# Kernel optimization log

Hardware: AMD Instinct MI355X
Metric: run time of the kernel (lower is better)

Reference implementation:

```python
import jax, jax.numpy as jnp
import numpy as np

N_EMBD = 768
N_HEAD = 12
HEAD_DIM = N_EMBD // N_HEAD
EPS = 1e-6


def setup_inputs() -> dict:
    key = jax.random.key(0)
    ks = jax.random.split(key, 8)
    B, T, C = 4, 2048, N_EMBD
    s = 0.02
    return {
        "x": jax.random.normal(ks[0], (B, T, C), jnp.float32),
        "ln1_w": jnp.ones((C,), jnp.float32),
        "ln1_b": jnp.zeros((C,), jnp.float32),
        "W_attn": jax.random.normal(ks[1], (C, 3 * C), jnp.float32) * s,
        "b_attn": jnp.zeros((3 * C,), jnp.float32),
        "W_attn_proj": jax.random.normal(ks[2], (C, C), jnp.float32) * s,
        "b_attn_proj": jnp.zeros((C,), jnp.float32),
        "ln2_w": jnp.ones((C,), jnp.float32),
        "ln2_b": jnp.zeros((C,), jnp.float32),
        "W_fc": jax.random.normal(ks[3], (C, 4 * C), jnp.float32) * s,
        "b_fc": jnp.zeros((4 * C,), jnp.float32),
        "W_mlp_proj": jax.random.normal(ks[4], (4 * C, C), jnp.float32) * s,
        "b_mlp_proj": jnp.zeros((C,), jnp.float32),
    }


def layer_norm(x, w, b):
    # Faithful to MyLayerNorm: (x - mean) / (std + eps), std with ddof=0
    mean = jnp.mean(x, axis=-1, keepdims=True)
    std = jnp.sqrt(jnp.mean((x - mean) ** 2, axis=-1, keepdims=True))
    return w * (x - mean) / (std + EPS) + b


def attention(h, W_attn, b_attn, W_proj, b_proj):
    B, T, C = h.shape
    qkv = h @ W_attn + b_attn                      # [B,T,3C]
    q, k, v = jnp.split(qkv, 3, axis=-1)
    # [B,T,C] -> [B,H,T,D]
    def to_heads(t):
        return t.reshape(B, T, N_HEAD, HEAD_DIM).transpose(0, 2, 1, 3)
    q, k, v = to_heads(q), to_heads(k), to_heads(v)
    att = jnp.einsum("bhtd,bhsd->bhts", q, k) * (1.0 / np.sqrt(HEAD_DIM))
    causal = jnp.tril(jnp.ones((T, T), bool))[None, None]
    att = jnp.where(causal, att, -jnp.inf)
    att = jax.nn.softmax(att, axis=-1)
    y = jnp.einsum("bhts,bhsd->bhtd", att, v)      # [B,H,T,D]
    y = y.transpose(0, 2, 1, 3).reshape(B, T, C)
    return y @ W_proj + b_proj


def mlp(h, W_fc, b_fc, W_proj, b_proj):
    h = jax.nn.gelu(h @ W_fc + b_fc, approximate=False)
    return h @ W_proj + b_proj


def reference(x, ln1_w, ln1_b, W_attn, b_attn, W_attn_proj, b_attn_proj,
              ln2_w, ln2_b, W_fc, b_fc, W_mlp_proj, b_mlp_proj):
    x = x + attention(layer_norm(x, ln1_w, ln1_b), W_attn, b_attn, W_attn_proj, b_attn_proj)
    x = x + mlp(layer_norm(x, ln2_w, ln2_b), W_fc, b_fc, W_mlp_proj, b_mlp_proj)
    return x
```

## Files before the change

### kernel.cpp

```cpp
#include <hip/hip_runtime.h>
#include <hip/hip_bf16.h>
#include <math.h>

#define N_EMBD 768
#define N_HEAD 12
#define HEAD_DIM 64
#define TOKENS 8192
#define SEQ 2048
#define BATCH 4
#define NQT (SEQ / 64)

typedef __attribute__((ext_vector_type(8))) short short8;
typedef __attribute__((ext_vector_type(4))) short short4v;
typedef __attribute__((ext_vector_type(4))) float f32x4;

__device__ __forceinline__ short f2bf(float f) {
    unsigned u = __builtin_bit_cast(unsigned, f);
    unsigned r = (u + 0x7fffu + ((u >> 16) & 1u)) >> 16;
    return (short)r;
}
__device__ __forceinline__ short f2bf_fast(float f) {
    unsigned u = __builtin_bit_cast(unsigned, f);
    return (short)((u + 0x8000u) >> 16);
}

__device__ __forceinline__ float gelu_fast(float x) {
    float z = 1.5957691216057308f * x * (1.0f + 0.044715f * x * x);
    return x / (1.0f + __expf(-z));
}

__device__ __forceinline__ void gld16(const void* g, void* l) {
    __builtin_amdgcn_global_load_lds(
        (const __attribute__((address_space(1))) unsigned int*)g,
        (__attribute__((address_space(3))) unsigned int*)l, 16, 0, 0);
}

__global__ __launch_bounds__(256) void wT_all(
        const float* __restrict__ Wa, short* __restrict__ Ta,
        const float* __restrict__ Wp, short* __restrict__ Tp,
        const float* __restrict__ Wf, short* __restrict__ Tf,
        const float* __restrict__ Wm, short* __restrict__ Tm) {
    __shared__ float T[32][33];
    int id = blockIdx.x;
    const float* W; short* Wt; int K, N;
    if (id < 1728)      { W = Wa; Wt = Ta; K = 768;  N = 2304; }
    else if (id < 2304) { W = Wp; Wt = Tp; K = 768;  N = 768;  id -= 1728; }
    else if (id < 4608) { W = Wf; Wt = Tf; K = 768;  N = 3072; id -= 2304; }
    else                { W = Wm; Wt = Tm; K = 3072; N = 768;  id -= 4608; }
    int tn = N >> 5;
    int n0 = (id % tn) * 32, k0 = (id / tn) * 32;
    int c = threadIdx.x & 31, r0 = threadIdx.x >> 5;
#pragma unroll
    for (int i = 0; i < 32; i += 8)
        T[r0 + i][c] = W[(size_t)(k0 + r0 + i) * N + n0 + c];
    __syncthreads();
#pragma unroll
    for (int i = 0; i < 32; i += 8)
        Wt[(size_t)(n0 + r0 + i) * K + k0 + c] = f2bf(T[c][r0 + i]);
}

__global__ __launch_bounds__(256) void ln_bf_kernel(const float* __restrict__ x,
                                                    const float* __restrict__ w,
                                                    const float* __restrict__ b,
                                                    short* __restrict__ out) {
    int row = blockIdx.x * 4 + (threadIdx.x >> 6);
    int lane = threadIdx.x & 63;
    const float4* xr = (const float4*)(x + (size_t)row * N_EMBD);
    const float4* wr = (const float4*)w;
    const float4* br = (const float4*)b;

    float4 v[3];
#pragma unroll
    for (int i = 0; i < 3; ++i) v[i] = xr[lane + 64 * i];
    float s = 0.f;
#pragma unroll
    for (int i = 0; i < 3; ++i) s += v[i].x + v[i].y + v[i].z + v[i].w;
#pragma unroll
    for (int off = 1; off < 64; off <<= 1) s += __shfl_xor(s, off, 64);
    float mean = s * (1.f / 768.f);

    float var = 0.f;
#pragma unroll
    for (int i = 0; i < 3; ++i) {
        float a0 = v[i].x - mean, a1 = v[i].y - mean,
              a2 = v[i].z - mean, a3 = v[i].w - mean;
        var += a0 * a0 + a1 * a1 + a2 * a2 + a3 * a3;
    }
#pragma unroll
    for (int off = 1; off < 64; off <<= 1) var += __shfl_xor(var, off, 64);
    float inv = 1.f / (sqrtf(var * (1.f / 768.f)) + 1e-6f);

    short4v* yr = (short4v*)(out + (size_t)row * N_EMBD);
#pragma unroll
    for (int i = 0; i < 3; ++i) {
        float4 wv = wr[lane + 64 * i], bv = br[lane + 64 * i];
        short4v o;
        o[0] = f2bf(wv.x * (v[i].x - mean) * inv + bv.x);
        o[1] = f2bf(wv.y * (v[i].y - mean) * inv + bv.y);
        o[2] = f2bf(wv.z * (v[i].z - mean) * inv + bv.z);
        o[3] = f2bf(wv.w * (v[i].w - mean) * inv + bv.w);
        yr[lane + 64 * i] = o;
    }
}

template <int ACT, int RES, int OUTBF, int VOUT>
__global__ __launch_bounds__(256) void gemm_mfma(
        const short* __restrict__ A,
        const short* __restrict__ Bt,
        const float* __restrict__ bias,
        const float* __restrict__ res,
        void* __restrict__ outp,
        short* __restrict__ vt,
        int M, int N, int K) {
    __shared__ short As[8192];
    __shared__ short Bs[8192];
    int tid = threadIdx.x;
    int wave = tid >> 6, lane = tid & 63;
    int quad = lane >> 4, l15 = lane & 15;
    int m0 = blockIdx.x * 128, n0 = blockIdx.y * 128;
    int wm = wave >> 1, wn = wave & 1;
    int sr = lane >> 2, sc = (lane & 3) * 8;

    f32x4 acc[4][4];
#pragma unroll
    for (int i = 0; i < 4; ++i)
#pragma unroll
        for (int j = 0; j < 4; ++j) acc[i][j] = (f32x4){0.f, 0.f, 0.f, 0.f};

    const short* ag = A + (size_t)(m0 + wave * 32 + sr) * K + sc;
    const short* bg = Bt + (size_t)(n0 + wave * 32 + sr) * K + sc;
    int woff = wave * 1024;

    gld16(ag, &As[woff]);
    gld16(ag + (size_t)16 * K, &As[woff + 512]);
    gld16(bg, &Bs[woff]);
    gld16(bg + (size_t)16 * K, &Bs[woff + 512]);

    int nk = K >> 5;
    for (int it = 0; it < nk; ++it) {
        int cb = (it & 1) * 4096;
        __syncthreads();
        if (it + 1 < nk) {
            int nb = ((it + 1) & 1) * 4096 + woff;
            int kn = (it + 1) << 5;
            gld16(ag + kn, &As[nb]);
            gld16(ag + kn + (size_t)16 * K, &As[nb + 512]);
            gld16(bg + kn, &Bs[nb]);
            gld16(bg + kn + (size_t)16 * K, &Bs[nb + 512]);
        }
        short8 af[4], bfr[4];
#pragma unroll
        for (int mt = 0; mt < 4; ++mt)
            af[mt] = *(const short8*)&As[cb + (wm * 64 + mt * 16 + l15) * 32 + quad * 8];
#pragma unroll
        for (int nt = 0; nt < 4; ++nt)
            bfr[nt] = *(const short8*)&Bs[cb + (wn * 64 + nt * 16 + l15) * 32 + quad * 8];
#pragma unroll
        for (int mt = 0; mt < 4; ++mt)
#pragma unroll
            for (int nt = 0; nt < 4; ++nt)
                acc[mt][nt] = __builtin_amdgcn_mfma_f32_16x16x32_bf16(
                    af[mt], bfr[nt], acc[mt][nt], 0, 0, 0);
    }

    if (VOUT && n0 >= 1536) {
#pragma unroll
        for (int mt = 0; mt < 4; ++mt) {
            int row0 = m0 + wm * 64 + mt * 16 + quad * 4;
            int b = row0 >> 11, t0 = row0 & 2047;
#pragma unroll
            for (int nt = 0; nt < 4; ++nt) {
                int col = n0 + wn * 64 + nt * 16 + l15;
                int vcol = col - 1536;
                int bh = b * N_HEAD + (vcol >> 6);
                int d = vcol & 63;
                float bi = bias[col];
                short4v o;
#pragma unroll
                for (int r = 0; r < 4; ++r) o[r] = f2bf(acc[mt][nt][r] + bi);
                *(short4v*)&vt[((size_t)bh * 64 + d) * SEQ + t0] = o;
            }
        }
        return;
    }

#pragma unroll
    for (int mt = 0; mt < 4; ++mt) {
        int row0 = m0 + wm * 64 + mt * 16 + quad * 4;
#pragma unroll
        for (int nt = 0; nt < 4; ++nt) {
            int col = n0 + wn * 64 + nt * 16 + l15;
            float bi = bias[col];
#pragma unroll
            for (int r = 0; r < 4; ++r) {
                float v = acc[mt][nt][r] + bi;
                if (ACT == 1) v = gelu_fast(v);
                if (RES) v += res[(size_t)(row0 + r) * N + col];
                if (OUTBF) ((short*)outp)[(size_t)(row0 + r) * N + col] = f2bf(v);
                else       ((float*)outp)[(size_t)(row0 + r) * N + col] = v;
            }
        }
    }
}

template <int ACT, int RES, int OUTBF>
__global__ __launch_bounds__(256) void gemm_mfma_n64(
        const short* __restrict__ A,
        const short* __restrict__ Bt,
        const float* __restrict__ bias,
        const float* __restrict__ res,
        void* __restrict__ outp,
        int M, int N, int K) {
    __shared__ short As[8192];
    __shared__ short Bs[4096];
    int tid = threadIdx.x;
    int wave = tid >> 6, lane = tid & 63;
    int quad = lane >> 4, l15 = lane & 15;
    int m0 = blockIdx.x * 128, n0 = blockIdx.y * 64;
    int wm = wave >> 1, wn = wave & 1;
    int sr = lane >> 2, sc = (lane & 3) * 8;

    f32x4 acc[4][2];
#pragma unroll
    for (int i = 0; i < 4; ++i)
#pragma unroll
        for (int j = 0; j < 2; ++j) acc[i][j] = (f32x4){0.f, 0.f, 0.f, 0.f};

    const short* gptr[3];
    int loff[3];
    bool isa[3];
#pragma unroll
    for (int j = 0; j < 3; ++j) {
        int c = wave * 3 + j;
        if (c < 8) {
            gptr[j] = A + (size_t)(m0 + c * 16 + sr) * K + sc;
            loff[j] = c * 512; isa[j] = true;
        } else {
            gptr[j] = Bt + (size_t)(n0 + (c - 8) * 16 + sr) * K + sc;
            loff[j] = (c - 8) * 512; isa[j] = false;
        }
    }

#pragma unroll
    for (int j = 0; j < 3; ++j)
        gld16(gptr[j], isa[j] ? &As[loff[j]] : &Bs[loff[j]]);

    int nk = K >> 5;
    for (int it = 0; it < nk; ++it) {
        int cba = (it & 1) * 4096, cbb = (it & 1) * 2048;
        __syncthreads();
        if (it + 1 < nk) {
            int nba = ((it + 1) & 1) * 4096, nbb = ((it + 1) & 1) * 2048;
            int kn = (it + 1) << 5;
#pragma unroll
            for (int j = 0; j < 3; ++j)
                gld16(gptr[j] + kn, isa[j] ? &As[nba + loff[j]] : &Bs[nbb + loff[j]]);
        }
        short8 af[4], bfr[2];
#pragma unroll
        for (int mt = 0; mt < 4; ++mt)
            af[mt] = *(const short8*)&As[cba + (wm * 64 + mt * 16 + l15) * 32 + quad * 8];
#pragma unroll
        for (int nt = 0; nt < 2; ++nt)
            bfr[nt] = *(const short8*)&Bs[cbb + (wn * 32 + nt * 16 + l15) * 32 + quad * 8];
#pragma unroll
        for (int mt = 0; mt < 4; ++mt)
#pragma unroll
            for (int nt = 0; nt < 2; ++nt)
                acc[mt][nt] = __builtin_amdgcn_mfma_f32_16x16x32_bf16(
                    af[mt], bfr[nt], acc[mt][nt], 0, 0, 0);
    }

#pragma unroll
    for (int mt = 0; mt < 4; ++mt) {
        int row0 = m0 + wm * 64 + mt * 16 + quad * 4;
#pragma unroll
        for (int nt = 0; nt < 2; ++nt) {
            int col = n0 + wn * 32 + nt * 16 + l15;
            float bi = bias[col];
#pragma unroll
            for (int r = 0; r < 4; ++r) {
                float v = acc[mt][nt][r] + bi;
                if (ACT == 1) v = gelu_fast(v);
                if (RES) v += res[(size_t)(row0 + r) * N + col];
                if (OUTBF) ((short*)outp)[(size_t)(row0 + r) * N + col] = f2bf(v);
                else       ((float*)outp)[(size_t)(row0 + r) * N + col] = v;
            }
        }
    }
}

__device__ __forceinline__ void attn_tile(
        const short* __restrict__ qkv, const short* __restrict__ Vt,
        short* __restrict__ y, int bh, int qt,
        short* Qs, short* Ks, short* Vs, short* Ps) {
    int tid = threadIdx.x;
    int wave = tid >> 6, lane = tid & 63;
    int quad = lane >> 4, l15 = lane & 15;
    int h = bh % N_HEAD, b = bh / N_HEAD;
    size_t bT = (size_t)b * SEQ;
    int q0 = qt * 64;
    int sr = lane >> 2, sc = (lane & 3) * 8;

    const short ONE_BF = (short)0x3F80;
    short8 ones;
#pragma unroll
    for (int j = 0; j < 8; ++j) ones[j] = ONE_BF;

    __syncthreads();
#pragma unroll
    for (int j = 0; j < 2; ++j) {
        int c = wave * 2 + j;
        int sub = c >> 2, r0 = (c & 3) * 16;
        const short* g = qkv + (bT + q0 + r0 + sr) * 2304 + h * 64 + sub * 32 + sc;
        gld16(g, &Qs[sub * 2048 + r0 * 32]);
    }
#pragma unroll
    for (int j = 0; j < 4; ++j) {
        int c = wave * 4 + j;
        if (c < 8) {
            int sub = c >> 2, r0 = (c & 3) * 16;
            const short* g = qkv + (bT + r0 + sr) * 2304 + 768 + h * 64 + sub * 32 + sc;
            gld16(g, &Ks[sub * 2048 + r0 * 32]);
        } else {
            int cv = c - 8;
            int sub = cv >> 2, r0 = (cv & 3) * 16;
            const short* g = Vt + ((size_t)bh * 64 + r0 + sr) * SEQ + sub * 32 + sc;
            gld16(g, &Vs[sub * 2048 + r0 * 32]);
        }
    }
    __syncthreads();
    short8 qf[2];
    qf[0] = *(const short8*)&Qs[(wave * 16 + l15) * 32 + quad * 8];
    qf[1] = *(const short8*)&Qs[2048 + (wave * 16 + l15) * 32 + quad * 8];

    f32x4 o[4];
#pragma unroll
    for (int nt = 0; nt < 4; ++nt) o[nt] = (f32x4){0.f, 0.f, 0.f, 0.f};
    f32x4 lacc = (f32x4){0.f, 0.f, 0.f, 0.f};

    for (int kt = 0; kt <= qt; ++kt) {
        int cb = (kt & 1) * 4096;
        if (kt) __syncthreads();
        if (kt < qt) {
            int nb = ((kt + 1) & 1) * 4096;
            int k0n = (kt + 1) * 64;
#pragma unroll
            for (int j = 0; j < 4; ++j) {
                int c = wave * 4 + j;
                if (c < 8) {
                    int sub = c >> 2, r0 = (c & 3) * 16;
                    const short* g = qkv + (bT + k0n + r0 + sr) * 2304 + 768 + h * 64 + sub * 32 + sc;
                    gld16(g, &Ks[nb + sub * 2048 + r0 * 32]);
                } else {
                    int cv = c - 8;
                    int sub = cv >> 2, r0 = (cv & 3) * 16;
                    const short* g = Vt + ((size_t)bh * 64 + r0 + sr) * SEQ + k0n + sub * 32 + sc;
                    gld16(g, &Vs[nb + sub * 2048 + r0 * 32]);
                }
            }
        }

        f32x4 sacc[4];
#pragma unroll
        for (int nt = 0; nt < 4; ++nt) sacc[nt] = (f32x4){0.f, 0.f, 0.f, 0.f};
#pragma unroll
        for (int nt = 0; nt < 4; ++nt)
#pragma unroll
            for (int ks = 0; ks < 2; ++ks) {
                short8 kf = *(const short8*)&Ks[cb + ks * 2048 + (nt * 16 + l15) * 32 + quad * 8];
                sacc[nt] = __builtin_amdgcn_mfma_f32_16x16x32_bf16(qf[ks], kf, sacc[nt], 0, 0, 0);
            }

        bool diag = (kt == qt);
#pragma unroll
        for (int nt = 0; nt < 4; ++nt) {
            int scol = nt * 16 + l15;
            int base = (scol >> 5) * 2048 + (scol & 31);
#pragma unroll
            for (int r = 0; r < 4; ++r) {
                float s = sacc[nt][r] * 0.125f - 4.0f;
                if (diag && (scol > wave * 16 + quad * 4 + r)) s = -1e30f;
                Ps[base + (wave * 16 + quad * 4 + r) * 32] = f2bf_fast(__expf(s));
            }
        }

        short8 pf0 = *(const short8*)&Ps[(wave * 16 + l15) * 32 + quad * 8];
        short8 pf1 = *(const short8*)&Ps[2048 + (wave * 16 + l15) * 32 + quad * 8];
        lacc = __builtin_amdgcn_mfma_f32_16x16x32_bf16(pf0, ones, lacc, 0, 0, 0);
        lacc = __builtin_amdgcn_mfma_f32_16x16x32_bf16(pf1, ones, lacc, 0, 0, 0);
#pragma unroll
        for (int nt = 0; nt < 4; ++nt) {
            short8 vf0 = *(const short8*)&Vs[cb + (nt * 16 + l15) * 32 + quad * 8];
            short8 vf1 = *(const short8*)&Vs[cb + 2048 + (nt * 16 + l15) * 32 + quad * 8];
            o[nt] = __builtin_amdgcn_mfma_f32_16x16x32_bf16(pf0, vf0, o[nt], 0, 0, 0);
            o[nt] = __builtin_amdgcn_mfma_f32_16x16x32_bf16(pf1, vf1, o[nt], 0, 0, 0);
        }
    }

    float inv[4];
#pragma unroll
    for (int r = 0; r < 4; ++r) inv[r] = 1.f / lacc[r];
#pragma unroll
    for (int nt = 0; nt < 4; ++nt)
#pragma unroll
        for (int r = 0; r < 4; ++r)
            y[(bT + q0 + wave * 16 + quad * 4 + r) * N_EMBD + h * 64 + nt * 16 + l15] =
                f2bf(o[nt][r] * inv[r]);
}

__global__ __launch_bounds__(256) void attn_mfma(
        const short* __restrict__ qkv, const short* __restrict__ Vt,
        short* __restrict__ y) {
    __shared__ short Qs[4096], Ks[8192], Vs[8192], Ps[4096];
    int bh = blockIdx.x;
    int pair = blockIdx.y;
    attn_tile(qkv, Vt, y, bh, pair, Qs, Ks, Vs, Ps);
    attn_tile(qkv, Vt, y, bh, NQT - 1 - pair, Qs, Ks, Vs, Ps);
}

extern "C" void kernel_launch(void* const* d_in, const int* in_sizes, int n_in,
                              void* d_out, int out_size, void* d_ws, size_t ws_size,
                              hipStream_t stream) {
    const float* x         = (const float*)d_in[0];
    const float* ln1_w     = (const float*)d_in[1];
    const float* ln1_b     = (const float*)d_in[2];
    const float* W_attn    = (const float*)d_in[3];
    const float* b_attn    = (const float*)d_in[4];
    const float* W_attn_pr = (const float*)d_in[5];
    const float* b_attn_pr = (const float*)d_in[6];
    const float* ln2_w     = (const float*)d_in[7];
    const float* ln2_b     = (const float*)d_in[8];
    const float* W_fc      = (const float*)d_in[9];
    const float* b_fc      = (const float*)d_in[10];
    const float* W_mlp_pr  = (const float*)d_in[11];
    const float* b_mlp_pr  = (const float*)d_in[12];
    float* out = (float*)d_out;

    const int M = TOKENS, C = N_EMBD;
    char* ws = (char*)d_ws;
    size_t region0 = (size_t)M * 3072 * 2;
    short* qkv_bf = (short*)ws;
    short* fc_bf  = (short*)ws;
    size_t off = region0;
    short* VtB   = (short*)(ws + off); off += (size_t)48 * 64 * SEQ * 2;
    short* yb    = (short*)(ws + off); off += (size_t)M * C * 2;
    short* lnb   = (short*)(ws + off); off += (size_t)M * C * 2;
    float* x1    = (float*)(ws + off); off += (size_t)M * C * 4;
    short* WaT   = (short*)(ws + off); off += (size_t)2304 * 768 * 2;
    short* WpT   = (short*)(ws + off); off += (size_t)768 * 768 * 2;
    short* WfT   = (short*)(ws + off); off += (size_t)3072 * 768 * 2;
    short* WmT   = (short*)(ws + off); off += (size_t)768 * 3072 * 2;

    wT_all<<<6912, 256, 0, stream>>>(W_attn, WaT, W_attn_pr, WpT,
                                     W_fc, WfT, W_mlp_pr, WmT);

    ln_bf_kernel<<<M / 4, 256, 0, stream>>>(x, ln1_w, ln1_b, lnb);

    gemm_mfma<0, 0, 1, 1><<<dim3(M / 128, 2304 / 128), 256, 0, stream>>>(
        lnb, WaT, b_attn, nullptr, qkv_bf, VtB, M, 2304, 768);

    attn_mfma<<<dim3(BATCH * N_HEAD, NQT / 2), 256, 0, stream>>>(qkv_bf, VtB, yb);

    gemm_mfma_n64<0, 1, 0><<<dim3(M / 128, 768 / 64), 256, 0, stream>>>(
        yb, WpT, b_attn_pr, x, x1, M, 768, 768);

    ln_bf_kernel<<<M / 4, 256, 0, stream>>>(x1, ln2_w, ln2_b, lnb);

    gemm_mfma<1, 0, 1, 0><<<dim3(M / 128, 3072 / 128), 256, 0, stream>>>(
        lnb, WfT, b_fc, nullptr, fc_bf, nullptr, M, 3072, 768);

    gemm_mfma_n64<0, 1, 0><<<dim3(M / 128, 768 / 64), 256, 0, stream>>>(
        fc_bf, WmT, b_mlp_pr, x1, out, M, 768, 3072);
}
```

Measured before the change: 367.9 us.

## Replace 128x128 GEMM with 256x256 eight-wave phased pipeline; swizzle attention P buffer

The QKV and FC GEMMs move from a 128x128, 4-wave double-buffered kernel to a 256x256, 8-wave kernel with a 64-wide K step. Each K iteration is split into four phases: quarter-tiles are prefetched asynchronously while MFMAs run between barriers, using explicit waitcnt, sched_barrier and setprio. The goal is more data reuse per LDS load and better overlap of global loads with compute. Separately, the attention P scratch buffer gets an XOR swizzle to reduce LDS bank conflicts. The larger tiles mean 128 KB of LDS and heavy register use per block, which can reduce occupancy, and the grids become smaller (for QKV, 32x9 blocks).

```diff
diff --git a/kernel.cpp b/kernel.cpp
--- a/kernel.cpp
+++ b/kernel.cpp
@@ -103,81 +103,133 @@
     }
 }
 
-template <int ACT, int RES, int OUTBF, int VOUT>
-__global__ __launch_bounds__(256) void gemm_mfma(
+template <int ACT, int VOUT>
+__global__ __launch_bounds__(512) void gemm_8ph(
         const short* __restrict__ A,
         const short* __restrict__ Bt,
         const float* __restrict__ bias,
-        const float* __restrict__ res,
-        void* __restrict__ outp,
+        short* __restrict__ outp,
         short* __restrict__ vt,
         int M, int N, int K) {
-    __shared__ short As[8192];
-    __shared__ short Bs[8192];
-    int tid = threadIdx.x;
-    int wave = tid >> 6, lane = tid & 63;
-    int quad = lane >> 4, l15 = lane & 15;
-    int m0 = blockIdx.x * 128, n0 = blockIdx.y * 128;
-    int wm = wave >> 1, wn = wave & 1;
-    int sr = lane >> 2, sc = (lane & 3) * 8;
-
-    f32x4 acc[4][4];
-#pragma unroll
-    for (int i = 0; i < 4; ++i)
+    __shared__ short lds[65536];
+    const int tid = threadIdx.x;
+    const int wid = tid >> 6, lane = tid & 63;
+    const int l15 = lane & 15, quad = lane >> 4;
+    const int wm = wid >> 2, wn = wid & 3;
+    const int m_blk = blockIdx.x * 256, n_blk = blockIdx.y * 256;
+    const int lo8 = lane << 3;
+
+    f32x4 acc[8][4];
+#pragma unroll
+    for (int i = 0; i < 8; ++i)
 #pragma unroll
         for (int j = 0; j < 4; ++j) acc[i][j] = (f32x4){0.f, 0.f, 0.f, 0.f};
 
-    const short* ag = A + (size_t)(m0 + wave * 32 + sr) * K + sc;
-    const short* bg = Bt + (size_t)(n0 + wave * 32 + sr) * K + sc;
-    int woff = wave * 1024;
-
-    gld16(ag, &As[woff]);
-    gld16(ag + (size_t)16 * K, &As[woff + 512]);
-    gld16(bg, &Bs[woff]);
-    gld16(bg + (size_t)16 * K, &Bs[woff + 512]);
-
-    int nk = K >> 5;
-    for (int it = 0; it < nk; ++it) {
-        int cb = (it & 1) * 4096;
-        __syncthreads();
-        if (it + 1 < nk) {
-            int nb = ((it + 1) & 1) * 4096 + woff;
-            int kn = (it + 1) << 5;
-            gld16(ag + kn, &As[nb]);
-            gld16(ag + kn + (size_t)16 * K, &As[nb + 512]);
-            gld16(bg + kn, &Bs[nb]);
-            gld16(bg + kn + (size_t)16 * K, &Bs[nb + 512]);
-        }
-        short8 af[4], bfr[4];
-#pragma unroll
-        for (int mt = 0; mt < 4; ++mt)
-            af[mt] = *(const short8*)&As[cb + (wm * 64 + mt * 16 + l15) * 32 + quad * 8];
-#pragma unroll
-        for (int nt = 0; nt < 4; ++nt)
-            bfr[nt] = *(const short8*)&Bs[cb + (wn * 64 + nt * 16 + l15) * 32 + quad * 8];
-#pragma unroll
-        for (int mt = 0; mt < 4; ++mt)
-#pragma unroll
-            for (int nt = 0; nt < 4; ++nt)
-                acc[mt][nt] = __builtin_amdgcn_mfma_f32_16x16x32_bf16(
-                    af[mt], bfr[nt], acc[mt][nt], 0, 0, 0);
-    }
-
-    if (VOUT && n0 >= 1536) {
-#pragma unroll
-        for (int mt = 0; mt < 4; ++mt) {
-            int row0 = m0 + wm * 64 + mt * 16 + quad * 4;
+    const int NT = K >> 6;
+
+    auto stagef = [&](int kt, int q) {
+        const int bufb = (kt & 1) << 15;
+        const short* gb = (q < 2) ? A : Bt;
+        int rbase = (q < 2) ? (m_blk + (q << 7)) : (n_blk + ((q - 2) << 7));
+        const short* src = gb + (size_t)(rbase + wid * 16 + l15) * K
+                           + (kt << 6) + quad * 8;
+        int lbase = bufb + ((q < 2) ? (q << 13) : (16384 + ((q - 2) << 13)))
+                    + (wid << 10);
+        gld16(src,      &lds[lbase]);
+        gld16(src + 32, &lds[lbase + 512]);
+    };
+
+    stagef(0, 0); stagef(0, 1); stagef(0, 2); stagef(0, 3);
+    stagef(1, 0); stagef(1, 1);
+    asm volatile("s_waitcnt vmcnt(4)" ::: "memory");
+    __builtin_amdgcn_s_barrier();
+
+#define PH_MID() do {                                        \
+        __builtin_amdgcn_s_barrier();                        \
+        asm volatile("s_waitcnt lgkmcnt(0)" ::: "memory");   \
+        __builtin_amdgcn_sched_barrier(0);                   \
+        __builtin_amdgcn_s_setprio(1); } while (0)
+#define PH_END() do {                                        \
+        __builtin_amdgcn_s_setprio(0);                       \
+        __builtin_amdgcn_s_barrier(); } while (0)
+
+    for (int t = 0; t < NT; ++t) {
+        const int bb = (t & 1) << 15;
+        const int aBase = bb + (wm << 13) + lo8;
+        const int bBase = bb + 16384 + ((wn >> 1) << 13) + ((wn & 1) << 12) + lo8;
+        short8 a0[8], a1[8], b0[4], b1[4];
+
+#pragma unroll
+        for (int m = 0; m < 8; ++m) a0[m] = *(const short8*)&lds[aBase + (m << 10)];
+#pragma unroll
+        for (int n = 0; n < 4; ++n) b0[n] = *(const short8*)&lds[bBase + (n << 10)];
+        if (t + 1 < NT) stagef(t + 1, 2);
+        PH_MID();
+#pragma unroll
+        for (int m = 0; m < 4; ++m)
+#pragma unroll
+            for (int n = 0; n < 4; ++n)
+                acc[m][n] = __builtin_amdgcn_mfma_f32_16x16x32_bf16(
+                    a0[m], b0[n], acc[m][n], 0, 0, 0);
+        PH_END();
+
+#pragma unroll
+        for (int m = 0; m < 8; ++m) a1[m] = *(const short8*)&lds[aBase + (m << 10) + 512];
+        if (t + 1 < NT) stagef(t + 1, 3);
+        PH_MID();
+#pragma unroll
+        for (int m = 0; m < 4; ++m)
+#pragma unroll
+            for (int n = 0; n < 4; ++n)
+                acc[m + 4][n] = __builtin_amdgcn_mfma_f32_16x16x32_bf16(
+                    a0[m + 4], b0[n], acc[m + 4][n], 0, 0, 0);
+        PH_END();
+
+#pragma unroll
+        for (int n = 0; n < 4; ++n) b1[n] = *(const short8*)&lds[bBase + (n << 10) + 512];
+        if (t + 2 < NT) stagef(t + 2, 0);
+        PH_MID();
+#pragma unroll
+        for (int m = 0; m < 4; ++m)
+#pragma unroll
+            for (int n = 0; n < 4; ++n)
+                acc[m][n] = __builtin_amdgcn_mfma_f32_16x16x32_bf16(
+                    a1[m], b1[n], acc[m][n], 0, 0, 0);
+        PH_END();
+
+        if (t + 2 < NT) {
+            stagef(t + 2, 1);
+            asm volatile("s_waitcnt vmcnt(4)" ::: "memory");
+        } else {
+            asm volatile("s_waitcnt vmcnt(0)" ::: "memory");
+        }
+        PH_MID();
+#pragma unroll
+        for (int m = 0; m < 4; ++m)
+#pragma unroll
+            for (int n = 0; n < 4; ++n)
+                acc[m + 4][n] = __builtin_amdgcn_mfma_f32_16x16x32_bf16(
+                    a1[m + 4], b1[n], acc[m + 4][n], 0, 0, 0);
+        PH_END();
+    }
+#undef PH_MID
+#undef PH_END
+
+    if (VOUT && n_blk >= 1536) {
+#pragma unroll
+        for (int m = 0; m < 8; ++m) {
+            int row0 = m_blk + wm * 128 + m * 16 + quad * 4;
             int b = row0 >> 11, t0 = row0 & 2047;
 #pragma unroll
-            for (int nt = 0; nt < 4; ++nt) {
-                int col = n0 + wn * 64 + nt * 16 + l15;
+            for (int n = 0; n < 4; ++n) {
+                int col = n_blk + wn * 64 + n * 16 + l15;
                 int vcol = col - 1536;
                 int bh = b * N_HEAD + (vcol >> 6);
                 int d = vcol & 63;
                 float bi = bias[col];
                 short4v o;
 #pragma unroll
-                for (int r = 0; r < 4; ++r) o[r] = f2bf(acc[mt][nt][r] + bi);
+                for (int r = 0; r < 4; ++r) o[r] = f2bf(acc[m][n][r] + bi);
                 *(short4v*)&vt[((size_t)bh * 64 + d) * SEQ + t0] = o;
             }
         }
@@ -185,19 +237,17 @@
     }
 
 #pragma unroll
-    for (int mt = 0; mt < 4; ++mt) {
-        int row0 = m0 + wm * 64 + mt * 16 + quad * 4;
-#pragma unroll
-        for (int nt = 0; nt < 4; ++nt) {
-            int col = n0 + wn * 64 + nt * 16 + l15;
+    for (int m = 0; m < 8; ++m) {
+        int row0 = m_blk + wm * 128 + m * 16 + quad * 4;
+#pragma unroll
+        for (int n = 0; n < 4; ++n) {
+            int col = n_blk + wn * 64 + n * 16 + l15;
             float bi = bias[col];
 #pragma unroll
             for (int r = 0; r < 4; ++r) {
-                float v = acc[mt][nt][r] + bi;
-                if (ACT == 1) v = gelu_fast(v);
-                if (RES) v += res[(size_t)(row0 + r) * N + col];
-                if (OUTBF) ((short*)outp)[(size_t)(row0 + r) * N + col] = f2bf(v);
-                else       ((float*)outp)[(size_t)(row0 + r) * N + col] = v;
+                float v = acc[m][n][r] + bi;
+                if (ACT) v = gelu_fast(v);
+                outp[(size_t)(row0 + r) * N + col] = f2bf(v);
             }
         }
     }
@@ -339,6 +389,8 @@
     for (int nt = 0; nt < 4; ++nt) o[nt] = (f32x4){0.f, 0.f, 0.f, 0.f};
     f32x4 lacc = (f32x4){0.f, 0.f, 0.f, 0.f};
 
+    const int pswz = ((l15 >> 2) & 3) << 4;
+
     for (int kt = 0; kt <= qt; ++kt) {
         int cb = (kt & 1) * 4096;
         if (kt) __syncthreads();
@@ -381,12 +433,13 @@
             for (int r = 0; r < 4; ++r) {
                 float s = sacc[nt][r] * 0.125f - 4.0f;
                 if (diag && (scol > wave * 16 + quad * 4 + r)) s = -1e30f;
-                Ps[base + (wave * 16 + quad * 4 + r) * 32] = f2bf_fast(__expf(s));
+                Ps[(base + (wave * 16 + quad * 4 + r) * 32) ^ (quad << 4)] =
+                    f2bf_fast(__expf(s));
             }
         }
 
-        short8 pf0 = *(const short8*)&Ps[(wave * 16 + l15) * 32 + quad * 8];
-        short8 pf1 = *(const short8*)&Ps[2048 + (wave * 16 + l15) * 32 + quad * 8];
+        short8 pf0 = *(const short8*)&Ps[((wave * 16 + l15) * 32 + quad * 8) ^ pswz];
+        short8 pf1 = *(const short8*)&Ps[(2048 + (wave * 16 + l15) * 32 + quad * 8) ^ pswz];
         lacc = __builtin_amdgcn_mfma_f32_16x16x32_bf16(pf0, ones, lacc, 0, 0, 0);
         lacc = __builtin_amdgcn_mfma_f32_16x16x32_bf16(pf1, ones, lacc, 0, 0, 0);
 #pragma unroll
@@ -457,8 +510,8 @@
 
     ln_bf_kernel<<<M / 4, 256, 0, stream>>>(x, ln1_w, ln1_b, lnb);
 
-    gemm_mfma<0, 0, 1, 1><<<dim3(M / 128, 2304 / 128), 256, 0, stream>>>(
-        lnb, WaT, b_attn, nullptr, qkv_bf, VtB, M, 2304, 768);
+    gemm_8ph<0, 1><<<dim3(M / 256, 2304 / 256), 512, 0, stream>>>(
+        lnb, WaT, b_attn, qkv_bf, VtB, M, 2304, 768);
 
     attn_mfma<<<dim3(BATCH * N_HEAD, NQT / 2), 256, 0, stream>>>(qkv_bf, VtB, yb);
 
@@ -467,8 +520,8 @@
 
     ln_bf_kernel<<<M / 4, 256, 0, stream>>>(x1, ln2_w, ln2_b, lnb);
 
-    gemm_mfma<1, 0, 1, 0><<<dim3(M / 128, 3072 / 128), 256, 0, stream>>>(
-        lnb, WfT, b_fc, nullptr, fc_bf, nullptr, M, 3072, 768);
+    gemm_8ph<1, 0><<<dim3(M / 256, 3072 / 256), 512, 0, stream>>>(
+        lnb, WfT, b_fc, fc_bf, nullptr, M, 3072, 768);
 
     gemm_mfma_n64<0, 1, 0><<<dim3(M / 128, 768 / 64), 256, 0, stream>>>(
         fc_bf, WmT, b_mlp_pr, x1, out, M, 768, 3072);
```

After: 392.4 us. +6.6%, slower.

## Restructure attention inner loop: peel diagonal tile, swizzle P, load Q directly

Applied to the files above, without the earlier changes.

The attention kernel now loads Q fragments straight from global memory into registers and drops the Q shared buffer. The key-tile loop is split into a templated helper so the causal-mask check is compiled only into the last (diagonal) tile, and the prefetch branch disappears from the main loop. The exp is rewritten as a single fma plus exp2, masked entries are set to zero directly, and the P tile in shared memory gets an XOR swizzle to reduce bank conflicts. Launch bounds now request 4 blocks per CU, which may force register limits and cause spills.

```diff
diff --git a/kernel.cpp b/kernel.cpp
--- a/kernel.cpp
+++ b/kernel.cpp
@@ -290,10 +290,54 @@
     }
 }
 
+template <bool DIAG>
+__device__ __forceinline__ void attn_kt(
+        const short* __restrict__ Ks, const short* __restrict__ Vs,
+        short* __restrict__ Ps, int cb,
+        const short8* qf, short8 ones,
+        f32x4* o, f32x4& lacc,
+        int wave, int quad, int l15, int pswz) {
+    f32x4 sacc[4];
+#pragma unroll
+    for (int nt = 0; nt < 4; ++nt) sacc[nt] = (f32x4){0.f, 0.f, 0.f, 0.f};
+#pragma unroll
+    for (int nt = 0; nt < 4; ++nt)
+#pragma unroll
+        for (int ks = 0; ks < 2; ++ks) {
+            short8 kf = *(const short8*)&Ks[cb + ks * 2048 + (nt * 16 + l15) * 32 + quad * 8];
+            sacc[nt] = __builtin_amdgcn_mfma_f32_16x16x32_bf16(qf[ks], kf, sacc[nt], 0, 0, 0);
+        }
+
+#pragma unroll
+    for (int nt = 0; nt < 4; ++nt) {
+        int scol = nt * 16 + l15;
+        int base = (scol >> 5) * 2048 + (scol & 31);
+#pragma unroll
+        for (int r = 0; r < 4; ++r) {
+            float p = exp2f(fmaf(sacc[nt][r], 0.18033688011112042f,
+                                 -5.770780163555854f));
+            if (DIAG && (scol > wave * 16 + quad * 4 + r)) p = 0.f;
+            Ps[(base + (wave * 16 + quad * 4 + r) * 32) ^ (quad << 4)] = f2bf_fast(p);
+        }
+    }
+
+    short8 pf0 = *(const short8*)&Ps[((wave * 16 + l15) * 32 + quad * 8) ^ pswz];
+    short8 pf1 = *(const short8*)&Ps[(2048 + (wave * 16 + l15) * 32 + quad * 8) ^ pswz];
+    lacc = __builtin_amdgcn_mfma_f32_16x16x32_bf16(pf0, ones, lacc, 0, 0, 0);
+    lacc = __builtin_amdgcn_mfma_f32_16x16x32_bf16(pf1, ones, lacc, 0, 0, 0);
+#pragma unroll
+    for (int nt = 0; nt < 4; ++nt) {
+        short8 vf0 = *(const short8*)&Vs[cb + (nt * 16 + l15) * 32 + quad * 8];
+        short8 vf1 = *(const short8*)&Vs[cb + 2048 + (nt * 16 + l15) * 32 + quad * 8];
+        o[nt] = __builtin_amdgcn_mfma_f32_16x16x32_bf16(pf0, vf0, o[nt], 0, 0, 0);
+        o[nt] = __builtin_amdgcn_mfma_f32_16x16x32_bf16(pf1, vf1, o[nt], 0, 0, 0);
+    }
+}
+
 __device__ __forceinline__ void attn_tile(
         const short* __restrict__ qkv, const short* __restrict__ Vt,
         short* __restrict__ y, int bh, int qt,
-        short* Qs, short* Ks, short* Vs, short* Ps) {
+        short* Ks, short* Vs, short* Ps) {
     int tid = threadIdx.x;
     int wave = tid >> 6, lane = tid & 63;
     int quad = lane >> 4, l15 = lane & 15;
@@ -307,14 +351,12 @@
 #pragma unroll
     for (int j = 0; j < 8; ++j) ones[j] = ONE_BF;
 
+    const short* qrow = qkv + (bT + q0 + wave * 16 + l15) * 2304 + h * 64 + quad * 8;
+    short8 qf[2];
+    qf[0] = *(const short8*)qrow;
+    qf[1] = *(const short8*)(qrow + 32);
+
     __syncthreads();
-#pragma unroll
-    for (int j = 0; j < 2; ++j) {
-        int c = wave * 2 + j;
-        int sub = c >> 2, r0 = (c & 3) * 16;
-        const short* g = qkv + (bT + q0 + r0 + sr) * 2304 + h * 64 + sub * 32 + sc;
-        gld16(g, &Qs[sub * 2048 + r0 * 32]);
-    }
 #pragma unroll
     for (int j = 0; j < 4; ++j) {
         int c = wave * 4 + j;
@@ -330,73 +372,39 @@
         }
     }
     __syncthreads();
-    short8 qf[2];
-    qf[0] = *(const short8*)&Qs[(wave * 16 + l15) * 32 + quad * 8];
-    qf[1] = *(const short8*)&Qs[2048 + (wave * 16 + l15) * 32 + quad * 8];
 
     f32x4 o[4];
 #pragma unroll
     for (int nt = 0; nt < 4; ++nt) o[nt] = (f32x4){0.f, 0.f, 0.f, 0.f};
     f32x4 lacc = (f32x4){0.f, 0.f, 0.f, 0.f};
 
-    for (int kt = 0; kt <= qt; ++kt) {
+    const int pswz = ((l15 >> 2) & 3) << 4;
+
+    for (int kt = 0; kt < qt; ++kt) {
         int cb = (kt & 1) * 4096;
         if (kt) __syncthreads();
-        if (kt < qt) {
-            int nb = ((kt + 1) & 1) * 4096;
-            int k0n = (kt + 1) * 64;
-#pragma unroll
-            for (int j = 0; j < 4; ++j) {
-                int c = wave * 4 + j;
-                if (c < 8) {
-                    int sub = c >> 2, r0 = (c & 3) * 16;
-                    const short* g = qkv + (bT + k0n + r0 + sr) * 2304 + 768 + h * 64 + sub * 32 + sc;
-                    gld16(g, &Ks[nb + sub * 2048 + r0 * 32]);
-                } else {
-                    int cv = c - 8;
-                    int sub = cv >> 2, r0 = (cv & 3) * 16;
-                    const short* g = Vt + ((size_t)bh * 64 + r0 + sr) * SEQ + k0n + sub * 32 + sc;
-                    gld16(g, &Vs[nb + sub * 2048 + r0 * 32]);
-                }
+        int nb = ((kt + 1) & 1) * 4096;
+        int k0n = (kt + 1) * 64;
+#pragma unroll
+        for (int j = 0; j < 4; ++j) {
+            int c = wave * 4 + j;
+            if (c < 8) {
+                int sub = c >> 2, r0 = (c & 3) * 16;
+                const short* g = qkv + (bT + k0n + r0 + sr) * 2304 + 768 + h * 64 + sub * 32 + sc;
+                gld16(g, &Ks[nb + sub * 2048 + r0 * 32]);
+            } else {
+                int cv = c - 8;
+                int sub = cv >> 2, r0 = (cv & 3) * 16;
+                const short* g = Vt + ((size_t)bh * 64 + r0 + sr) * SEQ + k0n + sub * 32 + sc;
+                gld16(g, &Vs[nb + sub * 2048 + r0 * 32]);
             }
         }
-
-        f32x4 sacc[4];
-#pragma unroll
-        for (int nt = 0; nt < 4; ++nt) sacc[nt] = (f32x4){0.f, 0.f, 0.f, 0.f};
-#pragma unroll
-        for (int nt = 0; nt < 4; ++nt)
-#pragma unroll
-            for (int ks = 0; ks < 2; ++ks) {
-                short8 kf = *(const short8*)&Ks[cb + ks * 2048 + (nt * 16 + l15) * 32 + quad * 8];
-                sacc[nt] = __builtin_amdgcn_mfma_f32_16x16x32_bf16(qf[ks], kf, sacc[nt], 0, 0, 0);
-            }
-
-        bool diag = (kt == qt);
-#pragma unroll
-        for (int nt = 0; nt < 4; ++nt) {
-            int scol = nt * 16 + l15;
-            int base = (scol >> 5) * 2048 + (scol & 31);
-#pragma unroll
-            for (int r = 0; r < 4; ++r) {
-                float s = sacc[nt][r] * 0.125f - 4.0f;
-                if (diag && (scol > wave * 16 + quad * 4 + r)) s = -1e30f;
-                Ps[base + (wave * 16 + quad * 4 + r) * 32] = f2bf_fast(__expf(s));
-            }
-        }
-
-        short8 pf0 = *(const short8*)&Ps[(wave * 16 + l15) * 32 + quad * 8];
-        short8 pf1 = *(const short8*)&Ps[2048 + (wave * 16 + l15) * 32 + quad * 8];
-        lacc = __builtin_amdgcn_mfma_f32_16x16x32_bf16(pf0, ones, lacc, 0, 0, 0);
-        lacc = __builtin_amdgcn_mfma_f32_16x16x32_bf16(pf1, ones, lacc, 0, 0, 0);
-#pragma unroll
-        for (int nt = 0; nt < 4; ++nt) {
-            short8 vf0 = *(const short8*)&Vs[cb + (nt * 16 + l15) * 32 + quad * 8];
-            short8 vf1 = *(const short8*)&Vs[cb + 2048 + (nt * 16 + l15) * 32 + quad * 8];
-            o[nt] = __builtin_amdgcn_mfma_f32_16x16x32_bf16(pf0, vf0, o[nt], 0, 0, 0);
-            o[nt] = __builtin_amdgcn_mfma_f32_16x16x32_bf16(pf1, vf1, o[nt], 0, 0, 0);
-        }
-    }
+        attn_kt<false>(Ks, Vs, Ps, cb, qf, ones, o, lacc, wave, quad, l15, pswz);
+    }
+
+    if (qt) __syncthreads();
+    attn_kt<true>(Ks, Vs, Ps, (qt & 1) * 4096, qf, ones, o, lacc,
+                  wave, quad, l15, pswz);
 
     float inv[4];
 #pragma unroll
@@ -409,14 +417,14 @@
                 f2bf(o[nt][r] * inv[r]);
 }
 
-__global__ __launch_bounds__(256) void attn_mfma(
+__global__ __launch_bounds__(256, 4) void attn_mfma(
         const short* __restrict__ qkv, const short* __restrict__ Vt,
         short* __restrict__ y) {
-    __shared__ short Qs[4096], Ks[8192], Vs[8192], Ps[4096];
+    __shared__ short Ks[8192], Vs[8192], Ps[4096];
     int bh = blockIdx.x;
     int pair = blockIdx.y;
-    attn_tile(qkv, Vt, y, bh, pair, Qs, Ks, Vs, Ps);
-    attn_tile(qkv, Vt, y, bh, NQT - 1 - pair, Qs, Ks, Vs, Ps);
+    attn_tile(qkv, Vt, y, bh, pair, Ks, Vs, Ps);
+    attn_tile(qkv, Vt, y, bh, NQT - 1 - pair, Ks, Vs, Ps);
 }
 
 extern "C" void kernel_launch(void* const* d_in, const int* in_sizes, int n_in,
```

Measured after the change: 370.5 us. Within noise of the previous version (+0.7%).
